# Kernel optimization log

Measured on AMD Instinct MI355X. Metric: run time of the kernel, lower is better.

## Reference

```python
import jax, jax.numpy as jnp
import numpy as np

D = 512
H = 8
FFN_H = 2048
NEG = -1.0e10


def layer_norm(x, gamma, beta, eps=1e-5):
    mu = jnp.mean(x, axis=-1, keepdims=True)
    var = jnp.var(x, axis=-1, keepdims=True)
    return (x - mu) * jax.lax.rsqrt(var + eps) * gamma + beta


def mha(x_q, x_kv, Wq, Wk, Wv, Wo, valid_lens):
    # x_q: [B,Tq,D], x_kv: [B,Tk,D]; valid_lens: [B,Tq] or [B]
    B, Tq, _ = x_q.shape
    Tk = x_kv.shape[1]
    dh = D // H
    q = (x_q @ Wq.T).reshape(B, Tq, H, dh).transpose(0, 2, 1, 3)  # [B,H,Tq,dh]
    k = (x_kv @ Wk.T).reshape(B, Tk, H, dh).transpose(0, 2, 1, 3)
    v = (x_kv @ Wv.T).reshape(B, Tk, H, dh).transpose(0, 2, 1, 3)
    scores = jnp.einsum('bhqd,bhkd->bhqk', q, k) / jnp.sqrt(jnp.float32(dh))
    pos = jnp.arange(Tk)
    if valid_lens.ndim == 1:  # [B] -> mask [B,1,1,Tk]
        mask = pos[None, None, None, :] < valid_lens[:, None, None, None]
    else:  # [B,Tq] -> mask [B,1,Tq,Tk]
        mask = pos[None, None, None, :] < valid_lens[:, None, :, None]
    scores = jnp.where(mask, scores, NEG)
    attn = jax.nn.softmax(scores, axis=-1)
    out = jnp.einsum('bhqk,bhkd->bhqd', attn, v)  # [B,H,Tq,dh]
    out = out.transpose(0, 2, 1, 3).reshape(B, Tq, D)
    return out @ Wo.T


def setup_inputs() -> dict:
    key = jax.random.key(0)
    ks = jax.random.split(key, 20)
    B, T = 32, 512
    s = 1.0 / np.sqrt(D)
    inp = {
        'X': jax.random.normal(ks[0], (B, T, D), jnp.float32),
        'enc_outputs': jax.random.normal(ks[1], (B, T, D), jnp.float32),
        'dec_valid_lens': jax.random.randint(ks[2], (B, T), 1, T + 1, jnp.int32),
        'enc_valid_lens': jax.random.randint(ks[3], (B,), 1, T + 1, jnp.int32),
    }
    names = ['Wq1', 'Wk1', 'Wv1', 'Wo1', 'Wq2', 'Wk2', 'Wv2', 'Wo2']
    for i, n in enumerate(names):
        inp[n] = jax.random.normal(ks[4 + i], (D, D), jnp.float32) * s
    inp['W1'] = jax.random.normal(ks[12], (FFN_H, D), jnp.float32) * s
    inp['b1'] = jnp.zeros((FFN_H,), jnp.float32)
    inp['W2'] = jax.random.normal(ks[13], (D, FFN_H), jnp.float32) * (1.0 / np.sqrt(FFN_H))
    inp['b2'] = jnp.zeros((D,), jnp.float32)
    for j in (1, 2, 3):
        inp[f'g{j}'] = jnp.ones((D,), jnp.float32)
        inp[f'be{j}'] = jnp.zeros((D,), jnp.float32)
    return inp


def reference(X, enc_outputs, dec_valid_lens, enc_valid_lens,
              Wq1, Wk1, Wv1, Wo1, Wq2, Wk2, Wv2, Wo2,
              W1, b1, W2, b2, g1, be1, g2, be2, g3, be3):
    # Training path: state[2][i] is None -> key_values = X. Dropout in eval mode (identity).
    X2 = mha(X, X, Wq1, Wk1, Wv1, Wo1, dec_valid_lens)            # self-attention
    Y = layer_norm(X + X2, g1, be1)                               # AddNorm1
    Y2 = mha(Y, enc_outputs, Wq2, Wk2, Wv2, Wo2, enc_valid_lens)  # cross-attention
    Z = layer_norm(Y + Y2, g2, be2)                               # AddNorm2
    F = (jax.nn.leaky_relu(Z @ W1.T + b1, 0.01)) @ W2.T + b2      # FFN (LeakyReLU slope 0.01)
    return layer_norm(Z + F, g3, be3)                             # AddNorm3
```

## Files before the change

kernel.cpp:

```cpp
#include <hip/hip_runtime.h>
#include <cstdint>
#include <cstddef>

typedef __bf16 bf16;
typedef __bf16 bf16x8 __attribute__((ext_vector_type(8)));
typedef float  f32x4  __attribute__((ext_vector_type(4)));
typedef unsigned short u16;

#define MD ((size_t)8388608)

__device__ __forceinline__ void async_copy16(const bf16* gp, bf16* lp) {
  __builtin_amdgcn_global_load_lds(
      (__attribute__((address_space(1))) void*)(gp),
      (__attribute__((address_space(3))) void*)(lp), 16, 0, 0);
}

__device__ __forceinline__ int is_f32(const u16* __restrict__ x) {
  const int e = (x[(threadIdx.x & 63) * 2] >> 7) & 0xFF;
  return __ballot(e >= 141) != 0ull;
}

struct ConvSrc { const void* p[20]; };

__global__ __launch_bounds__(256)
void convert_all(ConvSrc s, bf16* __restrict__ ws, const u16* __restrict__ xprobe)
{
  const int n[20] = {8388608, 8388608,
                     262144, 262144, 262144, 262144, 262144, 262144, 262144, 262144,
                     1048576, 2048, 1048576, 512, 512, 512, 512, 512, 512, 512};
  const unsigned int doff[20] = {
      41943040u, 50331648u,
      58720256u, 58982400u, 59244544u, 59506688u,
      59768832u, 60030976u, 60293120u, 60555264u,
      60817408u, 61865984u, 61868032u, 62916608u,
      62917120u, 62917632u, 62918144u, 62918656u, 62919168u, 62919680u};

  const int f32 = is_f32(xprobe);

  int bi = blockIdx.x;
  int idx = 0, b0 = 0;
  for (; idx < 20; ++idx) {
    const int nb = (n[idx] + 2047) >> 11;
    if (bi < b0 + nb) break;
    b0 += nb;
  }
  const int i = ((bi - b0) << 11) + threadIdx.x * 8;
  if (i >= n[idx]) return;
  bf16* dst = ws + doff[idx] + i;
  if (f32) {
    const float* sp = (const float*)s.p[idx] + i;
    f32x4 a = *(const f32x4*)sp;
    f32x4 b = *(const f32x4*)(sp + 4);
    bf16x8 o;
#pragma unroll
    for (int e = 0; e < 4; ++e) { o[e] = (bf16)a[e]; o[4 + e] = (bf16)b[e]; }
    *(bf16x8*)dst = o;
  } else {
    *(bf16x8*)dst = *(const bf16x8*)((const bf16*)s.p[idx] + i);
  }
}

template<int MODE, int TM, int TN>
__global__ __launch_bounds__(256)
void gemm_bt(const bf16* __restrict__ A, const bf16* __restrict__ B,
             const bf16* __restrict__ bias, bf16* __restrict__ C,
             int M, int N, int K)
{
  constexpr int MI = TM / 32;
  constexpr int NJ = TN / 32;
  constexpr int CA = TM / 32;
  constexpr int CB = TN / 32;
  __shared__ __attribute__((aligned(16))) bf16 As[TM * 64];
  __shared__ __attribute__((aligned(16))) bf16 Bs[TN * 64];

  const int t    = threadIdx.x;
  const int wave = t >> 6;
  const int lane = t & 63;
  const int quad = lane >> 4;
  const int l15  = lane & 15;
  const int wr   = (wave >> 1) * (TM / 2);
  const int wc   = (wave & 1) * (TN / 2);
  const int m0   = blockIdx.y * TM;
  const int n0   = blockIdx.x * TN;

  const bf16* gpa[CA];
  bf16*       lpa[CA];
#pragma unroll
  for (int c = 0; c < CA; ++c) {
    const int s   = c * 256 + t;
    const int row = s >> 3;
    const int kg  = ((s & 7) ^ (row & 7)) << 3;
    gpa[c] = A + (size_t)(m0 + row) * K + kg;
    lpa[c] = As + ((c * 256 + wave * 64) << 3);
  }
  const bf16* gpb[CB];
  bf16*       lpb[CB];
#pragma unroll
  for (int c = 0; c < CB; ++c) {
    const int s   = c * 256 + t;
    const int row = s >> 3;
    const int kg  = ((s & 7) ^ (row & 7)) << 3;
    gpb[c] = B + (size_t)(n0 + row) * K + kg;
    lpb[c] = Bs + ((c * 256 + wave * 64) << 3);
  }

  const f32x4 fz = {0.f, 0.f, 0.f, 0.f};
  f32x4 acc[MI][NJ];
#pragma unroll
  for (int i = 0; i < MI; ++i)
#pragma unroll
    for (int j = 0; j < NJ; ++j) acc[i][j] = fz;

  const int nkt = K >> 6;
  for (int kt = 0; kt < nkt; ++kt) {
    __syncthreads();
#pragma unroll
    for (int c = 0; c < CA; ++c) {
      async_copy16(gpa[c], lpa[c]);
      gpa[c] += 64;
    }
#pragma unroll
    for (int c = 0; c < CB; ++c) {
      async_copy16(gpb[c], lpb[c]);
      gpb[c] += 64;
    }
    __syncthreads();

#pragma unroll
    for (int ks = 0; ks < 2; ++ks) {
      bf16x8 af[MI], bfv[NJ];
#pragma unroll
      for (int i = 0; i < MI; ++i) {
        const int row = wr + i * 16 + l15;
        const int ph  = (ks * 4 + quad) ^ (row & 7);
        af[i] = *(const bf16x8*)(As + row * 64 + ph * 8);
      }
#pragma unroll
      for (int j = 0; j < NJ; ++j) {
        const int row = wc + j * 16 + l15;
        const int ph  = (ks * 4 + quad) ^ (row & 7);
        bfv[j] = *(const bf16x8*)(Bs + row * 64 + ph * 8);
      }
#pragma unroll
      for (int i = 0; i < MI; ++i)
#pragma unroll
        for (int j = 0; j < NJ; ++j)
          acc[i][j] = __builtin_amdgcn_mfma_f32_16x16x32_bf16(af[i], bfv[j],
                                                              acc[i][j], 0, 0, 0);
    }
  }

#pragma unroll
  for (int i = 0; i < MI; ++i) {
    const int m = m0 + wr + i * 16 + quad * 4;
#pragma unroll
    for (int j = 0; j < NJ; ++j) {
      const int n = n0 + wc + j * 16 + l15;
      float bv = 0.f;
      if (MODE >= 1) bv = (float)bias[n];
#pragma unroll
      for (int r = 0; r < 4; ++r) {
        float v = acc[i][j][r];
        if (MODE >= 1) v += bv;
        if (MODE == 1) v = v > 0.f ? v : 0.01f * v;
        C[(size_t)(m + r) * N + n] = (bf16)v;
      }
    }
  }
}

__global__ __launch_bounds__(256, 4)
void flash_attn(const bf16* __restrict__ Qp, const bf16* __restrict__ Kp,
                const bf16* __restrict__ Vp, bf16* __restrict__ Op,
                const int* __restrict__ vlen, int per_query, int sq, int skv)
{
  __shared__ __attribute__((aligned(16))) bf16 Ks[64][72];
  __shared__ __attribute__((aligned(16))) bf16 VsT[64][72];
  __shared__ __attribute__((aligned(16))) bf16 Ps[4][32][72];
  __shared__ int vlmax_sh;

  const int t    = threadIdx.x;
  const int wave = t >> 6;
  const int lane = t & 63;
  const int quad = lane >> 4;
  const int l15  = lane & 15;
  const int bx   = blockIdx.x;
  const int qt   = bx >> 8;
  const int h    = bx & 7;
  const int b    = (bx >> 3) & 31;
  const int q0   = qt * 128 + wave * 32;

  bf16x8 qfrag[2][2];
#pragma unroll
  for (int mt = 0; mt < 2; ++mt)
#pragma unroll
    for (int ks = 0; ks < 2; ++ks)
      qfrag[mt][ks] = *(const bf16x8*)(Qp +
          (size_t)(b * 512 + q0 + mt * 16 + l15) * sq + h * 64 + ks * 32 + quad * 8);

  int vl_r[2][4];
  int myvl = 1;
#pragma unroll
  for (int mt = 0; mt < 2; ++mt)
#pragma unroll
    for (int r = 0; r < 4; ++r) {
      const int q = q0 + mt * 16 + quad * 4 + r;
      const int v = per_query ? vlen[b * 512 + q] : vlen[b];
      vl_r[mt][r] = v;
      myvl = v > myvl ? v : myvl;
    }

  if (t == 0) vlmax_sh = 1;
  __syncthreads();
#pragma unroll
  for (int off = 1; off < 64; off <<= 1) {
    const int o = __shfl_xor(myvl, off);
    myvl = o > myvl ? o : myvl;
  }
  if (lane == 0) atomicMax(&vlmax_sh, myvl);
  __syncthreads();
  const int ktiles = (vlmax_sh + 63) >> 6;

  const f32x4 fz = {0.f, 0.f, 0.f, 0.f};
  float l_part[2][4] = {{0.f,0.f,0.f,0.f},{0.f,0.f,0.f,0.f}};
  f32x4 o_acc[2][4];
#pragma unroll
  for (int mt = 0; mt < 2; ++mt)
#pragma unroll
    for (int nt = 0; nt < 4; ++nt) o_acc[mt][nt] = fz;

  for (int kt = 0; kt < ktiles; ++kt) {
    const int k0 = kt * 64;
    __syncthreads();
    {
      const int r0 = t >> 3;
      const int c0 = (t & 7) * 8;
      const bf16* g = Kp + (size_t)(b * 512 + k0 + r0) * skv + h * 64 + c0;
      *(bf16x8*)&Ks[r0][c0]      = *(const bf16x8*)g;
      *(bf16x8*)&Ks[r0 + 32][c0] = *(const bf16x8*)(g + (size_t)32 * skv);
    }
    {
      const bf16* g = Vp + (size_t)(b * 512 + k0 + wave * 16) * skv + h * 64 + lane;
      bf16x8 lo, hi;
#pragma unroll
      for (int kk = 0; kk < 8; ++kk) lo[kk] = g[(size_t)kk * skv];
#pragma unroll
      for (int kk = 0; kk < 8; ++kk) hi[kk] = g[(size_t)(kk + 8) * skv];
      *(bf16x8*)&VsT[lane][wave * 16]     = lo;
      *(bf16x8*)&VsT[lane][wave * 16 + 8] = hi;
    }
    __syncthreads();

    f32x4 s[2][4];
#pragma unroll
    for (int mt = 0; mt < 2; ++mt)
#pragma unroll
      for (int nt = 0; nt < 4; ++nt) s[mt][nt] = fz;
#pragma unroll
    for (int ks = 0; ks < 2; ++ks)
#pragma unroll
      for (int nt = 0; nt < 4; ++nt) {
        const bf16x8 bk = *(const bf16x8*)&Ks[nt * 16 + l15][ks * 32 + quad * 8];
        s[0][nt] = __builtin_amdgcn_mfma_f32_16x16x32_bf16(qfrag[0][ks], bk, s[0][nt], 0, 0, 0);
        s[1][nt] = __builtin_amdgcn_mfma_f32_16x16x32_bf16(qfrag[1][ks], bk, s[1][nt], 0, 0, 0);
      }

#pragma unroll
    for (int mt = 0; mt < 2; ++mt)
#pragma unroll
      for (int nt = 0; nt < 4; ++nt) {
        const int k_abs = k0 + nt * 16 + l15;
#pragma unroll
        for (int r = 0; r < 4; ++r) {
          const float p = (k_abs < vl_r[mt][r]) ? __expf(s[mt][nt][r] * 0.125f) : 0.f;
          l_part[mt][r] += p;
          Ps[wave][mt * 16 + quad * 4 + r][nt * 16 + l15] = (bf16)p;
        }
      }

#pragma unroll
    for (int ks = 0; ks < 2; ++ks) {
      const bf16x8 ap0 = *(const bf16x8*)&Ps[wave][l15][ks * 32 + quad * 8];
      const bf16x8 ap1 = *(const bf16x8*)&Ps[wave][16 + l15][ks * 32 + quad * 8];
#pragma unroll
      for (int nt = 0; nt < 4; ++nt) {
        const bf16x8 bv = *(const bf16x8*)&VsT[nt * 16 + l15][ks * 32 + quad * 8];
        o_acc[0][nt] = __builtin_amdgcn_mfma_f32_16x16x32_bf16(ap0, bv, o_acc[0][nt], 0, 0, 0);
        o_acc[1][nt] = __builtin_amdgcn_mfma_f32_16x16x32_bf16(ap1, bv, o_acc[1][nt], 0, 0, 0);
      }
    }
  }

#pragma unroll
  for (int mt = 0; mt < 2; ++mt)
#pragma unroll
    for (int r = 0; r < 4; ++r) {
      float l = l_part[mt][r];
#pragma unroll
      for (int off = 1; off < 16; off <<= 1)
        l += __shfl_xor(l, off);
      const float inv_l = (l > 0.f) ? (1.f / l) : 0.f;
      const int q = q0 + mt * 16 + quad * 4 + r;
#pragma unroll
      for (int nt = 0; nt < 4; ++nt)
        Op[(size_t)(b * 512 + q) * 512 + h * 64 + nt * 16 + l15] =
            (bf16)(o_acc[mt][nt][r] * inv_l);
    }
}

__global__ __launch_bounds__(256)
void add_layernorm(const bf16* X, const bf16* R,
                   const bf16* __restrict__ gamma, const bf16* __restrict__ beta,
                   bf16* Out)
{
  const int t    = threadIdx.x;
  const int wave = t >> 6;
  const int lane = t & 63;
  const size_t row  = (size_t)blockIdx.x * 4 + wave;
  const size_t base = row * 512 + lane * 8;

  bf16x8 xv = *(const bf16x8*)(X + base);
  bf16x8 rv = *(const bf16x8*)(R + base);
  float v[8];
  float sum = 0.f, ss = 0.f;
#pragma unroll
  for (int i = 0; i < 8; ++i) {
    v[i] = (float)xv[i] + (float)rv[i];
    sum += v[i];
    ss  += v[i] * v[i];
  }
#pragma unroll
  for (int off = 1; off < 64; off <<= 1) {
    sum += __shfl_xor(sum, off);
    ss  += __shfl_xor(ss, off);
  }
  const float mean = sum * (1.f / 512.f);
  const float var  = ss * (1.f / 512.f) - mean * mean;
  const float rstd = rsqrtf(var + 1e-5f);

  bf16x8 gv = *(const bf16x8*)(gamma + lane * 8);
  bf16x8 bv = *(const bf16x8*)(beta + lane * 8);
  bf16x8 ov;
#pragma unroll
  for (int i = 0; i < 8; ++i)
    ov[i] = (bf16)(((v[i] - mean) * rstd) * (float)gv[i] + (float)bv[i]);
  *(bf16x8*)(Out + base) = ov;
}

__global__ __launch_bounds__(256)
void add_layernorm_out(const bf16* X, const bf16* R,
                       const bf16* __restrict__ gamma, const bf16* __restrict__ beta,
                       void* Out, const u16* __restrict__ xprobe)
{
  const int t    = threadIdx.x;
  const int wave = t >> 6;
  const int lane = t & 63;
  const size_t row  = (size_t)blockIdx.x * 4 + wave;
  const size_t base = row * 512 + lane * 8;

  const int f32 = is_f32(xprobe);

  bf16x8 xv = *(const bf16x8*)(X + base);
  bf16x8 rv = *(const bf16x8*)(R + base);
  float v[8];
  float sum = 0.f, ss = 0.f;
#pragma unroll
  for (int i = 0; i < 8; ++i) {
    v[i] = (float)xv[i] + (float)rv[i];
    sum += v[i];
    ss  += v[i] * v[i];
  }
#pragma unroll
  for (int off = 1; off < 64; off <<= 1) {
    sum += __shfl_xor(sum, off);
    ss  += __shfl_xor(ss, off);
  }
  const float mean = sum * (1.f / 512.f);
  const float var  = ss * (1.f / 512.f) - mean * mean;
  const float rstd = rsqrtf(var + 1e-5f);

  bf16x8 gv = *(const bf16x8*)(gamma + lane * 8);
  bf16x8 bv = *(const bf16x8*)(beta + lane * 8);
  float o[8];
#pragma unroll
  for (int i = 0; i < 8; ++i)
    o[i] = ((v[i] - mean) * rstd) * (float)gv[i] + (float)bv[i];

  if (f32) {
    float* op = (float*)Out + base;
    f32x4 o0 = {o[0], o[1], o[2], o[3]};
    f32x4 o1 = {o[4], o[5], o[6], o[7]};
    *(f32x4*)op       = o0;
    *(f32x4*)(op + 4) = o1;
  } else {
    bf16x8 ov;
#pragma unroll
    for (int i = 0; i < 8; ++i) ov[i] = (bf16)o[i];
    *(bf16x8*)((bf16*)Out + base) = ov;
  }
}

extern "C" void kernel_launch(void* const* d_in, const int* in_sizes, int n_in,
                              void* d_out, int out_size, void* d_ws, size_t ws_size,
                              hipStream_t stream)
{
  (void)in_sizes; (void)n_in; (void)out_size; (void)ws_size;

  const int* dvl = (const int*)d_in[2];
  const int* evl = (const int*)d_in[3];
  const u16* xprobe = (const u16*)d_in[0];

  bf16* ws = (bf16*)d_ws;
  bf16* S0 = ws;
  bf16* S1 = ws + 1 * MD;
  bf16* S3 = ws + 3 * MD;
  bf16* S4 = ws + 4 * MD;
  bf16* Xb = ws + 5 * MD;
  bf16* Eb = ws + 6 * MD;
  bf16* W  = ws + 7 * MD;
  const bf16 *Wq1 = W,
             *Wo1 = W + 786432,   *Wq2 = W + 1048576, *Wk2 = W + 1310720,
             *Wo2 = W + 1835008,
             *W1  = W + 2097152,  *b1  = W + 3145728,
             *W2  = W + 3147776,  *b2  = W + 4196352,
             *g1  = W + 4196864,  *be1 = W + 4197376,
             *g2  = W + 4197888,  *be2 = W + 4198400,
             *g3  = W + 4198912,  *be3 = W + 4199424;

  ConvSrc cs;
  cs.p[0] = d_in[0];  cs.p[1] = d_in[1];
  for (int k = 0; k < 12; ++k) cs.p[2 + k] = d_in[4 + k];
  for (int k = 0; k < 6; ++k)  cs.p[14 + k] = d_in[16 + k];
  convert_all<<<dim3(10248), dim3(256), 0, stream>>>(cs, ws, xprobe);

  dim3 blk(256);
  dim3 gP(4, 256);
  dim3 gQKV(12, 128);
  dim3 gKV(8, 128);
  dim3 gF1(16, 128);

  gemm_bt<0,128,128><<<gQKV, blk, 0, stream>>>(Xb, Wq1, nullptr, S0, 16384, 1536, 512);
  flash_attn<<<dim3(1024), blk, 0, stream>>>(S0, S0 + 512, S0 + 1024, S3, dvl, 1, 1536, 1536);
  gemm_bt<0,64,128><<<gP, blk, 0, stream>>>(S3, Wo1, nullptr, S1, 16384, 512, 512);
  add_layernorm<<<dim3(4096), blk, 0, stream>>>(Xb, S1, g1, be1, S4);

  gemm_bt<0,64,128><<<gP,  blk, 0, stream>>>(S4, Wq2, nullptr, S0, 16384, 512, 512);
  gemm_bt<0,128,128><<<gKV, blk, 0, stream>>>(Eb, Wk2, nullptr, S1, 16384, 1024, 512);
  flash_attn<<<dim3(1024), blk, 0, stream>>>(S0, S1, S1 + 512, S3, evl, 0, 512, 1024);
  gemm_bt<0,64,128><<<gP, blk, 0, stream>>>(S3, Wo2, nullptr, S1, 16384, 512, 512);
  add_layernorm<<<dim3(4096), blk, 0, stream>>>(S4, S1, g2, be2, S4);

  gemm_bt<1,128,128><<<gF1, blk, 0, stream>>>(S4, W1, b1, S0, 16384, 2048, 512);
  gemm_bt<2,64,128><<<gP,  blk, 0, stream>>>(S0, W2, b2, Xb, 16384, 512, 2048);
  add_layernorm_out<<<dim3(4096), blk, 0, stream>>>(S4, Xb, g3, be3, d_out, xprobe);
}
```

Before: 483.0 us.

## Fuse fp32-to-bf16 activation conversion into GEMM A loads and layernorm

Drops the separate conversion pass over X and enc_outputs. The QKV and cross-KV GEMMs now read the raw (possibly fp32) activations through registers, convert them to bf16, and store them into LDS. The first add-layernorm reads raw X directly. It also switches the N=512 GEMMs from 64x128 to 128x128 tiles, which halves their grid. This saves a full read and write of two 8M-element tensors, but the converted A path gives up async global-to-LDS copies, so load latency in those GEMMs may be less hidden.

Result: slower. 526.0 us (+8.9%).

```diff
diff --git a/kernel.cpp b/kernel.cpp
--- a/kernel.cpp
+++ b/kernel.cpp
@@ -20,16 +20,14 @@
   return __ballot(e >= 141) != 0ull;
 }
 
-struct ConvSrc { const void* p[20]; };
+struct ConvSrc { const void* p[18]; };
 
 __global__ __launch_bounds__(256)
 void convert_all(ConvSrc s, bf16* __restrict__ ws, const u16* __restrict__ xprobe)
 {
-  const int n[20] = {8388608, 8388608,
-                     262144, 262144, 262144, 262144, 262144, 262144, 262144, 262144,
+  const int n[18] = {262144, 262144, 262144, 262144, 262144, 262144, 262144, 262144,
                      1048576, 2048, 1048576, 512, 512, 512, 512, 512, 512, 512};
-  const unsigned int doff[20] = {
-      41943040u, 50331648u,
+  const unsigned int doff[18] = {
       58720256u, 58982400u, 59244544u, 59506688u,
       59768832u, 60030976u, 60293120u, 60555264u,
       60817408u, 61865984u, 61868032u, 62916608u,
@@ -39,7 +37,7 @@
 
   int bi = blockIdx.x;
   int idx = 0, b0 = 0;
-  for (; idx < 20; ++idx) {
+  for (; idx < 18; ++idx) {
     const int nb = (n[idx] + 2047) >> 11;
     if (bi < b0 + nb) break;
     b0 += nb;
@@ -60,11 +58,11 @@
   }
 }
 
-template<int MODE, int TM, int TN>
+template<int MODE, int TM, int TN, int AF32>
 __global__ __launch_bounds__(256)
-void gemm_bt(const bf16* __restrict__ A, const bf16* __restrict__ B,
+void gemm_bt(const void* __restrict__ Araw, const bf16* __restrict__ B,
              const bf16* __restrict__ bias, bf16* __restrict__ C,
-             int M, int N, int K)
+             int M, int N, int K, const u16* __restrict__ xprobe)
 {
   constexpr int MI = TM / 32;
   constexpr int NJ = TN / 32;
@@ -83,26 +81,8 @@
   const int m0   = blockIdx.y * TM;
   const int n0   = blockIdx.x * TN;
 
-  const bf16* gpa[CA];
-  bf16*       lpa[CA];
-#pragma unroll
-  for (int c = 0; c < CA; ++c) {
-    const int s   = c * 256 + t;
-    const int row = s >> 3;
-    const int kg  = ((s & 7) ^ (row & 7)) << 3;
-    gpa[c] = A + (size_t)(m0 + row) * K + kg;
-    lpa[c] = As + ((c * 256 + wave * 64) << 3);
-  }
-  const bf16* gpb[CB];
-  bf16*       lpb[CB];
-#pragma unroll
-  for (int c = 0; c < CB; ++c) {
-    const int s   = c * 256 + t;
-    const int row = s >> 3;
-    const int kg  = ((s & 7) ^ (row & 7)) << 3;
-    gpb[c] = B + (size_t)(n0 + row) * K + kg;
-    lpb[c] = Bs + ((c * 256 + wave * 64) << 3);
-  }
+  int af32 = 0;
+  if (AF32) af32 = is_f32(xprobe);
 
   const f32x4 fz = {0.f, 0.f, 0.f, 0.f};
   f32x4 acc[MI][NJ];
@@ -113,16 +93,50 @@
 
   const int nkt = K >> 6;
   for (int kt = 0; kt < nkt; ++kt) {
+    const int k0 = kt << 6;
+
+    bf16x8 areg[CA];
+    if (AF32) {
+#pragma unroll
+      for (int c = 0; c < CA; ++c) {
+        const int s   = c * 256 + t;
+        const int row = s >> 3;
+        const int kg  = ((s & 7) ^ (row & 7)) << 3;
+        if (af32) {
+          const float* g = (const float*)Araw + (size_t)(m0 + row) * K + k0 + kg;
+          f32x4 lo = *(const f32x4*)g;
+          f32x4 hi = *(const f32x4*)(g + 4);
+#pragma unroll
+          for (int e = 0; e < 4; ++e) { areg[c][e] = (bf16)lo[e]; areg[c][4 + e] = (bf16)hi[e]; }
+        } else {
+          areg[c] = *(const bf16x8*)((const bf16*)Araw + (size_t)(m0 + row) * K + k0 + kg);
+        }
+      }
+    }
+
     __syncthreads();
-#pragma unroll
-    for (int c = 0; c < CA; ++c) {
-      async_copy16(gpa[c], lpa[c]);
-      gpa[c] += 64;
+
+    if (AF32) {
+#pragma unroll
+      for (int c = 0; c < CA; ++c)
+        *(bf16x8*)(As + (size_t)(c * 256 + t) * 8) = areg[c];
+    } else {
+#pragma unroll
+      for (int c = 0; c < CA; ++c) {
+        const int s   = c * 256 + t;
+        const int row = s >> 3;
+        const int kg  = ((s & 7) ^ (row & 7)) << 3;
+        async_copy16((const bf16*)Araw + (size_t)(m0 + row) * K + k0 + kg,
+                     As + ((c * 256 + wave * 64) << 3));
+      }
     }
 #pragma unroll
     for (int c = 0; c < CB; ++c) {
-      async_copy16(gpb[c], lpb[c]);
-      gpb[c] += 64;
+      const int s   = c * 256 + t;
+      const int row = s >> 3;
+      const int kg  = ((s & 7) ^ (row & 7)) << 3;
+      async_copy16(B + (size_t)(n0 + row) * K + k0 + kg,
+                   Bs + ((c * 256 + wave * 64) << 3));
     }
     __syncthreads();
 
@@ -348,6 +362,57 @@
 }
 
 __global__ __launch_bounds__(256)
+void add_layernorm_x(const void* Xraw, const bf16* R,
+                     const bf16* __restrict__ gamma, const bf16* __restrict__ beta,
+                     bf16* Out, const u16* __restrict__ xprobe)
+{
+  const int t    = threadIdx.x;
+  const int wave = t >> 6;
+  const int lane = t & 63;
+  const size_t row  = (size_t)blockIdx.x * 4 + wave;
+  const size_t base = row * 512 + lane * 8;
+
+  const int f32 = is_f32(xprobe);
+
+  float v[8];
+  if (f32) {
+    const float* xp = (const float*)Xraw + base;
+    f32x4 a = *(const f32x4*)xp;
+    f32x4 b = *(const f32x4*)(xp + 4);
+#pragma unroll
+    for (int i = 0; i < 4; ++i) { v[i] = a[i]; v[4 + i] = b[i]; }
+  } else {
+    bf16x8 xv = *(const bf16x8*)((const bf16*)Xraw + base);
+#pragma unroll
+    for (int i = 0; i < 8; ++i) v[i] = (float)xv[i];
+  }
+  bf16x8 rv = *(const bf16x8*)(R + base);
+  float sum = 0.f, ss = 0.f;
+#pragma unroll
+  for (int i = 0; i < 8; ++i) {
+    v[i] += (float)rv[i];
+    sum += v[i];
+    ss  += v[i] * v[i];
+  }
+#pragma unroll
+  for (int off = 1; off < 64; off <<= 1) {
+    sum += __shfl_xor(sum, off);
+    ss  += __shfl_xor(ss, off);
+  }
+  const float mean = sum * (1.f / 512.f);
+  const float var  = ss * (1.f / 512.f) - mean * mean;
+  const float rstd = rsqrtf(var + 1e-5f);
+
+  bf16x8 gv = *(const bf16x8*)(gamma + lane * 8);
+  bf16x8 bv = *(const bf16x8*)(beta + lane * 8);
+  bf16x8 ov;
+#pragma unroll
+  for (int i = 0; i < 8; ++i)
+    ov[i] = (bf16)(((v[i] - mean) * rstd) * (float)gv[i] + (float)bv[i]);
+  *(bf16x8*)(Out + base) = ov;
+}
+
+__global__ __launch_bounds__(256)
 void add_layernorm_out(const bf16* X, const bf16* R,
                        const bf16* __restrict__ gamma, const bf16* __restrict__ beta,
                        void* Out, const u16* __restrict__ xprobe)
@@ -416,7 +481,6 @@
   bf16* S3 = ws + 3 * MD;
   bf16* S4 = ws + 4 * MD;
   bf16* Xb = ws + 5 * MD;
-  bf16* Eb = ws + 6 * MD;
   bf16* W  = ws + 7 * MD;
   const bf16 *Wq1 = W,
              *Wo1 = W + 786432,   *Wq2 = W + 1048576, *Wk2 = W + 1310720,
@@ -428,29 +492,28 @@
              *g3  = W + 4198912,  *be3 = W + 4199424;
 
   ConvSrc cs;
-  cs.p[0] = d_in[0];  cs.p[1] = d_in[1];
-  for (int k = 0; k < 12; ++k) cs.p[2 + k] = d_in[4 + k];
-  for (int k = 0; k < 6; ++k)  cs.p[14 + k] = d_in[16 + k];
-  convert_all<<<dim3(10248), dim3(256), 0, stream>>>(cs, ws, xprobe);
+  for (int k = 0; k < 12; ++k) cs.p[k] = d_in[4 + k];
+  for (int k = 0; k < 6; ++k)  cs.p[12 + k] = d_in[16 + k];
+  convert_all<<<dim3(2056), dim3(256), 0, stream>>>(cs, ws, xprobe);
 
   dim3 blk(256);
-  dim3 gP(4, 256);
+  dim3 gP(4, 128);
   dim3 gQKV(12, 128);
   dim3 gKV(8, 128);
   dim3 gF1(16, 128);
 
-  gemm_bt<0,128,128><<<gQKV, blk, 0, stream>>>(Xb, Wq1, nullptr, S0, 16384, 1536, 512);
+  gemm_bt<0,128,128,1><<<gQKV, blk, 0, stream>>>(d_in[0], Wq1, nullptr, S0, 16384, 1536, 512, xprobe);
   flash_attn<<<dim3(1024), blk, 0, stream>>>(S0, S0 + 512, S0 + 1024, S3, dvl, 1, 1536, 1536);
-  gemm_bt<0,64,128><<<gP, blk, 0, stream>>>(S3, Wo1, nullptr, S1, 16384, 512, 512);
-  add_layernorm<<<dim3(4096), blk, 0, stream>>>(Xb, S1, g1, be1, S4);
-
-  gemm_bt<0,64,128><<<gP,  blk, 0, stream>>>(S4, Wq2, nullptr, S0, 16384, 512, 512);
-  gemm_bt<0,128,128><<<gKV, blk, 0, stream>>>(Eb, Wk2, nullptr, S1, 16384, 1024, 512);
+  gemm_bt<0,128,128,0><<<gP, blk, 0, stream>>>(S3, Wo1, nullptr, S1, 16384, 512, 512, xprobe);
+  add_layernorm_x<<<dim3(4096), blk, 0, stream>>>(d_in[0], S1, g1, be1, S4, xprobe);
+
+  gemm_bt<0,128,128,0><<<gP,  blk, 0, stream>>>(S4, Wq2, nullptr, S0, 16384, 512, 512, xprobe);
+  gemm_bt<0,128,128,1><<<gKV, blk, 0, stream>>>(d_in[1], Wk2, nullptr, S1, 16384, 1024, 512, xprobe);
   flash_attn<<<dim3(1024), blk, 0, stream>>>(S0, S1, S1 + 512, S3, evl, 0, 512, 1024);
-  gemm_bt<0,64,128><<<gP, blk, 0, stream>>>(S3, Wo2, nullptr, S1, 16384, 512, 512);
+  gemm_bt<0,128,128,0><<<gP, blk, 0, stream>>>(S3, Wo2, nullptr, S1, 16384, 512, 512, xprobe);
   add_layernorm<<<dim3(4096), blk, 0, stream>>>(S4, S1, g2, be2, S4);
 
-  gemm_bt<1,128,128><<<gF1, blk, 0, stream>>>(S4, W1, b1, S0, 16384, 2048, 512);
-  gemm_bt<2,64,128><<<gP,  blk, 0, stream>>>(S0, W2, b2, Xb, 16384, 512, 2048);
+  gemm_bt<1,128,128,0><<<gF1, blk, 0, stream>>>(S4, W1, b1, S0, 16384, 2048, 512, xprobe);
+  gemm_bt<2,128,128,0><<<gP,  blk, 0, stream>>>(S0, W2, b2, Xb, 16384, 512, 2048, xprobe);
   add_layernorm_out<<<dim3(4096), blk, 0, stream>>>(S4, Xb, g3, be3, d_out, xprobe);
 }
```
